# Performance work log

Hardware: AMD Instinct MI355X
Metric: run time of the kernel (lower is better)

The kernel has to match this reference:

```python
import jax, jax.numpy as jnp
import numpy as np

B, S, D = 2, 2048, 1024
H = 16
HD = D // H  # 64


def setup_inputs() -> dict:
    key = jax.random.key(0)
    ks = jax.random.split(key, 9)
    s = 1.0 / np.sqrt(D)
    return {
        "query_input": jax.random.normal(ks[0], (B, S, D), dtype=jnp.float32),
        "Wq": jax.random.normal(ks[1], (D, D), dtype=jnp.float32) * s,
        "bq": jax.random.normal(ks[2], (D,), dtype=jnp.float32) * 0.02,
        "Wk": jax.random.normal(ks[3], (D, D), dtype=jnp.float32) * s,
        "bk": jax.random.normal(ks[4], (D,), dtype=jnp.float32) * 0.02,
        "Wv": jax.random.normal(ks[5], (D, D), dtype=jnp.float32) * s,
        "bv": jax.random.normal(ks[6], (D,), dtype=jnp.float32) * 0.02,
        "Wo": jax.random.normal(ks[7], (D, D), dtype=jnp.float32) * s,
        "bo": jax.random.normal(ks[8], (D,), dtype=jnp.float32) * 0.02,
    }


def _split_heads(x):
    # [B, S, D] -> [B, H, S, HD]
    return x.reshape(B, S, H, HD).transpose(0, 2, 1, 3)


def reference(query_input, Wq, bq, Wk, bk, Wv, bv, Wo, bo):
    # self-attention: key_value_input = query_input
    q = _split_heads(query_input @ Wq + bq)
    k = _split_heads(query_input @ Wk + bk)
    v = _split_heads(query_input @ Wv + bv)
    scores = jnp.einsum("bhqd,bhkd->bhqk", q, k) / jnp.sqrt(jnp.float32(HD))
    probs = jax.nn.softmax(scores, axis=-1)  # dropout is identity in eval
    ctx = jnp.einsum("bhqk,bhkd->bhqd", probs, v)
    ctx = ctx.transpose(0, 2, 1, 3).reshape(B, S, D)
    return ctx @ Wo + bo
```

## Files before the change

kernel.cpp:

```cpp
#include <hip/hip_runtime.h>
#include <hip/hip_bf16.h>
#include <cstdint>

constexpr int Bsz = 2, Seq = 2048, Dim = 1024, NH = 16, HDim = 64;
constexpr int Mtok = Bsz * Seq;
constexpr int NQKV = 3 * Dim;
constexpr float QSCALE = 0.125f * 1.4426950408889634f;

typedef __attribute__((ext_vector_type(4))) float f32x4;
typedef __attribute__((ext_vector_type(16))) float f32x16;
typedef __attribute__((ext_vector_type(8))) short bf16x8;

#if __has_builtin(__builtin_amdgcn_exp2f)
#define EXP2(x) __builtin_amdgcn_exp2f(x)
#else
#define EXP2(x) exp2f(x)
#endif

__device__ __forceinline__ ushort f2bf(float f) {
    union { float f; uint32_t u; } v; v.f = f;
    uint32_t u = v.u;
    uint32_t r = (u + 0x7fffu + ((u >> 16) & 1u)) >> 16;
    return (ushort)r;
}

__device__ __forceinline__ uint cvt_pk_bf16(float lo, float hi) {
    uint r;
    asm("v_cvt_pk_bf16_f32 %0, %1, %2" : "=v"(r) : "v"(lo), "v"(hi));
    return r;
}

__device__ __forceinline__ void gll16(const ushort* g, ushort* l) {
    __builtin_amdgcn_global_load_lds(
        (const __attribute__((address_space(1))) void*)g,
        (__attribute__((address_space(3))) void*)l, 16, 0, 0);
}

__global__ void convert_x(const float* __restrict__ in, ushort* __restrict__ out, int n16) {
    int i = blockIdx.x * 256 + threadIdx.x;
    if (i >= n16) return;
    int e = i * 16;
    int row = e >> 10;
    int k = e & 1023;
    int k0 = k & ~31;
    int c = (k >> 3) & 3;
    int sw = row & 3;
    const float4* p = (const float4*)(in + e);
    float4 a = p[0], b = p[1], c2 = p[2], d = p[3];
    uint4 o0, o1;
    o0.x = (uint)f2bf(a.x) | ((uint)f2bf(a.y) << 16);
    o0.y = (uint)f2bf(a.z) | ((uint)f2bf(a.w) << 16);
    o0.z = (uint)f2bf(b.x) | ((uint)f2bf(b.y) << 16);
    o0.w = (uint)f2bf(b.z) | ((uint)f2bf(b.w) << 16);
    o1.x = (uint)f2bf(c2.x) | ((uint)f2bf(c2.y) << 16);
    o1.y = (uint)f2bf(c2.z) | ((uint)f2bf(c2.w) << 16);
    o1.z = (uint)f2bf(d.x) | ((uint)f2bf(d.y) << 16);
    o1.w = (uint)f2bf(d.z) | ((uint)f2bf(d.w) << 16);
    ushort* dstrow = out + (size_t)row * 1024 + k0;
    *(uint4*)(dstrow + ((c ^ sw) << 3))       = o0;
    *(uint4*)(dstrow + (((c + 1) ^ sw) << 3)) = o1;
}

__global__ void transpose_w4(const float* __restrict__ Wq, const float* __restrict__ Wk,
                             const float* __restrict__ Wv, const float* __restrict__ Wo,
                             ushort* __restrict__ Wtqkv, ushort* __restrict__ Wto) {
    __shared__ float tile[32][33];
    int z = blockIdx.z;
    const float* src = (z == 0) ? Wq : (z == 1) ? Wk : (z == 2) ? Wv : Wo;
    ushort* dst = (z == 3) ? Wto : Wtqkv + (size_t)z * 1024 * 1024;
    float scale = (z == 0) ? QSCALE : 1.f;
    int bx = blockIdx.x * 32, by = blockIdx.y * 32;
    int tx = threadIdx.x, ty = threadIdx.y;
#pragma unroll
    for (int j = 0; j < 32; j += 8)
        tile[ty + j][tx] = src[(size_t)(by + ty + j) * Dim + bx + tx];
    __syncthreads();
    int c = tx >> 3, wn8 = tx & 7;
#pragma unroll
    for (int j = 0; j < 32; j += 8) {
        int n = bx + ty + j;
        dst[(size_t)n * Dim + by + ((c ^ (n & 3)) << 3) + wn8] = f2bf(tile[tx][ty + j] * scale);
    }
}

__global__ void concat_bias(const float* __restrict__ bq, const float* __restrict__ bk,
                            const float* __restrict__ bv, float* __restrict__ dst) {
    int i = blockIdx.x * 256 + threadIdx.x;
    if (i >= NQKV) return;
    float v = (i < 1024) ? bq[i] * QSCALE : (i < 2048 ? bk[i - 1024] : bv[i - 2048]);
    dst[i] = v;
}

__global__ __launch_bounds__(256) void gemm_qkv(const ushort* __restrict__ A,
                                                const ushort* __restrict__ Bt,
                                                const float* __restrict__ bias,
                                                ushort* __restrict__ Qp,
                                                ushort* __restrict__ Kp,
                                                ushort* __restrict__ Vp) {
    __shared__ ushort As[2][128 * 32];
    __shared__ ushort Bs[2][128 * 32];
    const int tid = threadIdx.x;
    const int lane = tid & 63, wid = tid >> 6;
    const int wm = wid >> 1, wn = wid & 1;
    const int bm = blockIdx.x * 128, bn = blockIdx.y * 128;
    const int g = lane >> 4, r16 = lane & 15;
    const int Ksz = Dim;

    f32x4 acc[4][4] = {};

    const int srow = tid >> 2;
    const int sc = tid & 3;
    const ushort* ga0 = A + (size_t)(bm + srow) * Ksz + sc * 8;
    const ushort* ga1 = A + (size_t)(bm + 64 + srow) * Ksz + sc * 8;
    const ushort* gb0 = Bt + (size_t)(bn + srow) * Ksz + sc * 8;
    const ushort* gb1 = Bt + (size_t)(bn + 64 + srow) * Ksz + sc * 8;
    const int lofs = wid << 9;

#define GSTAGE(bufi, k_)  do {                          \
        gll16(ga0 + (k_), &As[bufi][lofs]);             \
        gll16(ga1 + (k_), &As[bufi][2048 + lofs]);      \
        gll16(gb0 + (k_), &Bs[bufi][lofs]);             \
        gll16(gb1 + (k_), &Bs[bufi][2048 + lofs]);      \
    } while (0)

    GSTAGE(0, 0);
    int cur = 0;

    for (int k0 = 0; k0 < Ksz; k0 += 32) {
        __syncthreads();
        if (k0 + 32 < Ksz) GSTAGE(cur ^ 1, k0 + 32);
        const ushort* Asb = As[cur];
        const ushort* Bsb = Bs[cur];
        bf16x8 af[4], bfr[4];
#pragma unroll
        for (int mt = 0; mt < 4; mt++) {
            int row = wm * 64 + mt * 16 + r16;
            af[mt] = *(const bf16x8*)(Asb + row * 32 + ((g ^ (row & 3)) * 8));
        }
#pragma unroll
        for (int nt = 0; nt < 4; nt++) {
            int row = wn * 64 + nt * 16 + r16;
            bfr[nt] = *(const bf16x8*)(Bsb + row * 32 + ((g ^ (row & 3)) * 8));
        }
#pragma unroll
        for (int mt = 0; mt < 4; mt++)
#pragma unroll
            for (int nt = 0; nt < 4; nt++)
                acc[mt][nt] = __builtin_amdgcn_mfma_f32_16x16x32_bf16(af[mt], bfr[nt], acc[mt][nt], 0, 0, 0);
        cur ^= 1;
    }
#undef GSTAGE

#pragma unroll
    for (int nt = 0; nt < 4; nt++) {
        int col = bn + wn * 64 + nt * 16 + r16;
        float bv = bias[col];
        if (col < 1024) {
#pragma unroll
            for (int mt = 0; mt < 4; mt++) {
                int row0 = bm + wm * 64 + mt * 16 + g * 4;
                f32x4 c = acc[mt][nt];
#pragma unroll
                for (int i = 0; i < 4; i++)
                    Qp[(size_t)(row0 + i) * 1024 + col] = f2bf(c[i] + bv);
            }
        } else if (col < 2048) {
            int h = (col - 1024) >> 6, d = (col - 1024) & 63;
#pragma unroll
            for (int mt = 0; mt < 4; mt++) {
                int row0 = bm + wm * 64 + mt * 16 + g * 4;
                f32x4 c = acc[mt][nt];
#pragma unroll
                for (int i = 0; i < 4; i++) {
                    int row = row0 + i;
                    int b = row >> 11, s = row & 2047;
                    size_t idx = ((size_t)(b * 16 + h) * 2048 + s) * 64
                               + (((d >> 3) ^ (s & 7)) << 3) + (d & 7);
                    Kp[idx] = f2bf(c[i] + bv);
                }
            }
        } else {
            int h = (col - 2048) >> 6, dv = (col - 2048) & 63;
#pragma unroll
            for (int mt = 0; mt < 4; mt++) {
                int row0 = bm + wm * 64 + mt * 16 + g * 4;
                f32x4 c = acc[mt][nt];
                int b = row0 >> 11, s = row0 & 2047;
                int s0 = s & ~63, si = s & 63;
                uint2 pk;
                pk.x = cvt_pk_bf16(c[0] + bv, c[1] + bv);
                pk.y = cvt_pk_bf16(c[2] + bv, c[3] + bv);
                size_t idx = ((size_t)(b * 16 + h) * 2048 + s0) * 64 + dv * 64
                           + (((si >> 3) ^ (dv & 7)) << 3) + (si & 7);
                *(uint2*)(Vp + idx) = pk;
            }
        }
    }
}

__global__ __launch_bounds__(256) void gemm_bt(const ushort* __restrict__ A,
                                               const ushort* __restrict__ Bt,
                                               const float* __restrict__ bias,
                                               float* __restrict__ Cout,
                                               int Nsz, int Ksz) {
    __shared__ ushort As[2][128 * 32];
    __shared__ ushort Bs[2][128 * 32];
    const int tid = threadIdx.x;
    const int lane = tid & 63, wid = tid >> 6;
    const int wm = wid >> 1, wn = wid & 1;
    const int bm = blockIdx.x * 128, bn = blockIdx.y * 128;
    const int g = lane >> 4, r16 = lane & 15;

    f32x4 acc[4][4] = {};

    const int srow = tid >> 2;
    const int sc = tid & 3;
    const ushort* ga0 = A + (size_t)(bm + srow) * Ksz + sc * 8;
    const ushort* ga1 = A + (size_t)(bm + 64 + srow) * Ksz + sc * 8;
    const ushort* gb0 = Bt + (size_t)(bn + srow) * Ksz + sc * 8;
    const ushort* gb1 = Bt + (size_t)(bn + 64 + srow) * Ksz + sc * 8;
    const int lofs = wid << 9;

#define GSTAGE(bufi, k_)  do {                          \
        gll16(ga0 + (k_), &As[bufi][lofs]);             \
        gll16(ga1 + (k_), &As[bufi][2048 + lofs]);      \
        gll16(gb0 + (k_), &Bs[bufi][lofs]);             \
        gll16(gb1 + (k_), &Bs[bufi][2048 + lofs]);      \
    } while (0)

    GSTAGE(0, 0);
    int cur = 0;

    for (int k0 = 0; k0 < Ksz; k0 += 32) {
        __syncthreads();
        if (k0 + 32 < Ksz) GSTAGE(cur ^ 1, k0 + 32);
        const ushort* Asb = As[cur];
        const ushort* Bsb = Bs[cur];
        bf16x8 af[4], bfr[4];
#pragma unroll
        for (int mt = 0; mt < 4; mt++) {
            int row = wm * 64 + mt * 16 + r16;
            af[mt] = *(const bf16x8*)(Asb + row * 32 + ((g ^ (row & 3)) * 8));
        }
#pragma unroll
        for (int nt = 0; nt < 4; nt++) {
            int row = wn * 64 + nt * 16 + r16;
            bfr[nt] = *(const bf16x8*)(Bsb + row * 32 + ((g ^ (row & 3)) * 8));
        }
#pragma unroll
        for (int mt = 0; mt < 4; mt++)
#pragma unroll
            for (int nt = 0; nt < 4; nt++)
                acc[mt][nt] = __builtin_amdgcn_mfma_f32_16x16x32_bf16(af[mt], bfr[nt], acc[mt][nt], 0, 0, 0);
        cur ^= 1;
    }
#undef GSTAGE

#pragma unroll
    for (int nt = 0; nt < 4; nt++) {
        int col = bn + wn * 64 + nt * 16 + r16;
        float bv = bias[col];
#pragma unroll
        for (int mt = 0; mt < 4; mt++) {
            int row0 = bm + wm * 64 + mt * 16 + g * 4;
            f32x4 c = acc[mt][nt];
#pragma unroll
            for (int i = 0; i < 4; i++)
                Cout[(size_t)(row0 + i) * Nsz + col] = c[i] + bv;
        }
    }
}

__global__ __launch_bounds__(256) void attn(const ushort* __restrict__ Qp,
                                            const ushort* __restrict__ Kp,
                                            const ushort* __restrict__ Vp,
                                            ushort* __restrict__ Ctx) {
    __shared__ ushort Ks[2][64 * 64];
    __shared__ ushort Vs[2][64 * 64];
    __shared__ float Rl[4][32];
    const int tid = threadIdx.x, lane = tid & 63, w = tid >> 6;
    const int bh = blockIdx.y, b = bh >> 4, h = bh & 15;
    const int l31 = lane & 31, hi = lane >> 5, sw7 = l31 & 7;
    const bool lo = (hi == 0);
    const int qrow = blockIdx.x * 128 + w * 32;

    const ushort* Qr = Qp + (size_t)(b * Seq + qrow + l31) * 1024 + h * 64;
    bf16x8 qf[4];
#pragma unroll
    for (int ks = 0; ks < 4; ks++)
        qf[ks] = *(const bf16x8*)(Qr + ks * 16 + hi * 8);

    const ushort* KpB = Kp + (size_t)bh * Seq * 64;
    const ushort* VpB = Vp + (size_t)bh * Seq * 64;
    const int wb = w * 512;

#define STAGE(bufi, kv0_)  do {                                        \
        const ushort* ks_ = KpB + (size_t)(kv0_) * 64 + tid * 8;       \
        const ushort* vs_ = VpB + (size_t)(kv0_) * 64 + tid * 8;       \
        gll16(ks_,        &Ks[bufi][wb]);                              \
        gll16(ks_ + 2048, &Ks[bufi][2048 + wb]);                       \
        gll16(vs_,        &Vs[bufi][wb]);                              \
        gll16(vs_ + 2048, &Vs[bufi][2048 + wb]);                       \
    } while (0)

    STAGE(0, 0);

    f32x16 c0 = {}, c1 = {};
    float l_run = 0.f;
    int cur = 0;

    for (int kv0 = 0; kv0 < Seq; kv0 += 64) {
        __syncthreads();
        if (kv0 + 64 < Seq) STAGE(cur ^ 1, kv0 + 64);
        const ushort* Kt = Ks[cur];
        const ushort* Vt = Vs[cur];

        f32x16 s0, s1;
#pragma unroll
        for (int r = 0; r < 16; r++) { s0[r] = -8.f; s1[r] = -8.f; }
        __builtin_amdgcn_s_setprio(1);
#pragma unroll
        for (int ks = 0; ks < 4; ks++) {
            int ch = ((ks * 2 + hi) ^ sw7) << 3;
            bf16x8 k0 = *(const bf16x8*)(Kt + l31 * 64 + ch);
            bf16x8 k1 = *(const bf16x8*)(Kt + (32 + l31) * 64 + ch);
            s0 = __builtin_amdgcn_mfma_f32_32x32x16_bf16(k0, qf[ks], s0, 0, 0, 0);
            s1 = __builtin_amdgcn_mfma_f32_32x32x16_bf16(k1, qf[ks], s1, 0, 0, 0);
        }
        __builtin_amdgcn_s_setprio(0);

        float p0[16], p1[16];
        float ls0 = 0.f, ls1 = 0.f;
#pragma unroll
        for (int r = 0; r < 16; r++) {
            p0[r] = EXP2(s0[r]);
            p1[r] = EXP2(s1[r]);
            ls0 += p0[r]; ls1 += p1[r];
        }
        l_run += ls0 + ls1;

        bf16x8 pa[4];
#pragma unroll
        for (int sl = 0; sl < 4; sl++) {
            const float* pp = (sl < 2) ? p0 : p1;
            int rb = (sl & 1) * 8;
            uint x  = cvt_pk_bf16(pp[rb + 0], pp[rb + 1]);
            uint x2 = cvt_pk_bf16(pp[rb + 2], pp[rb + 3]);
            uint y  = cvt_pk_bf16(pp[rb + 4], pp[rb + 5]);
            uint y2 = cvt_pk_bf16(pp[rb + 6], pp[rb + 7]);
            asm("v_permlane32_swap_b32 %0, %1" : "+v"(x),  "+v"(y));
            asm("v_permlane32_swap_b32 %0, %1" : "+v"(x2), "+v"(y2));
            union { uint u[4]; bf16x8 v; } fr;
            fr.u[0] = x;
            fr.u[1] = x2;
            fr.u[2] = y;
            fr.u[3] = y2;
            pa[sl] = fr.v;
        }

        __builtin_amdgcn_s_setprio(1);
#pragma unroll
        for (int sl = 0; sl < 4; sl++) {
            int ch = ((sl * 2 + hi) ^ sw7) << 3;
            bf16x8 vf0 = *(const bf16x8*)(Vt + l31 * 64 + ch);
            bf16x8 vf1 = *(const bf16x8*)(Vt + (32 + l31) * 64 + ch);
            c0 = __builtin_amdgcn_mfma_f32_32x32x16_bf16(pa[sl], vf0, c0, 0, 0, 0);
            c1 = __builtin_amdgcn_mfma_f32_32x32x16_bf16(pa[sl], vf1, c1, 0, 0, 0);
        }
        __builtin_amdgcn_s_setprio(0);
        cur ^= 1;
    }
#undef STAGE

    float lt = l_run + __shfl_xor(l_run, 32);
    if (lo) Rl[w][l31] = 1.f / lt;
    __builtin_amdgcn_s_waitcnt(0);
    float rlv[16];
#pragma unroll
    for (int r = 0; r < 16; r++)
        rlv[r] = Rl[w][(r & 3) + 8 * (r >> 2) + 4 * hi];

    const int rowbase = b * Seq + qrow;
    const int cl = l31 >> 3, c7 = l31 & 7;
#pragma unroll
    for (int r = 0; r < 16; r++) {
        int q = (r & 3) + 8 * (r >> 2) + 4 * hi;
        int row = rowbase + q;
        int col0 = h * 64 + ((cl ^ (row & 3)) << 3) + c7;
        int col1 = h * 64 + 32 + ((cl ^ (row & 3)) << 3) + c7;
        Ctx[(size_t)row * Dim + col0] = f2bf(c0[r] * rlv[r]);
        Ctx[(size_t)row * Dim + col1] = f2bf(c1[r] * rlv[r]);
    }
}

extern "C" void kernel_launch(void* const* d_in, const int* in_sizes, int n_in,
                              void* d_out, int out_size, void* d_ws, size_t ws_size,
                              hipStream_t stream) {
    const float* X  = (const float*)d_in[0];
    const float* Wq = (const float*)d_in[1];
    const float* bq = (const float*)d_in[2];
    const float* Wk = (const float*)d_in[3];
    const float* bk = (const float*)d_in[4];
    const float* Wv = (const float*)d_in[5];
    const float* bv = (const float*)d_in[6];
    const float* Wo = (const float*)d_in[7];
    const float* bo = (const float*)d_in[8];

    char* ws = (char*)d_ws;
    ushort* Xb    = (ushort*)(ws);
    ushort* Wtqkv = (ushort*)(ws + 8388608);
    ushort* Wto   = (ushort*)(ws + 14680064);
    float*  bqkv  = (float*)(ws + 16777216);
    ushort* Qp    = (ushort*)(ws + 16793600);
    ushort* Kp    = (ushort*)(ws + 25182208);
    ushort* Vp    = (ushort*)(ws + 33570816);
    ushort* Ctxb  = (ushort*)(ws + 41959424);

    convert_x<<<1024, 256, 0, stream>>>(X, Xb, Mtok * Dim / 16);
    transpose_w4<<<dim3(32, 32, 4), dim3(32, 8), 0, stream>>>(Wq, Wk, Wv, Wo, Wtqkv, Wto);
    concat_bias<<<12, 256, 0, stream>>>(bq, bk, bv, bqkv);

    gemm_qkv<<<dim3(32, 24), 256, 0, stream>>>(Xb, Wtqkv, bqkv, Qp, Kp, Vp);
    attn<<<dim3(16, 32), 256, 0, stream>>>(Qp, Kp, Vp, Ctxb);
    gemm_bt<<<dim3(32, 8), 256, 0, stream>>>(Ctxb, Wto, bo, (float*)d_out, Dim, Dim);
}
```

Baseline: 130.6 us.

## Rewrite QKV GEMM with 256x256 tiles, 8 waves, and interleaved load/MFMA schedule

The QKV projection GEMM now uses 256x256 block tiles with 512 threads and a 64-wide K step. Global-to-LDS loads are split into A and B halves and issued between MFMA phases, with explicit barriers, priority hints and vmcnt waits. The XOR swizzle that producers used to apply to stored data is removed and applied instead on the global-load side of the GEMMs, so producers write plain row-major output. Larger tiles raise data reuse and cut the block count, but the grid of 192 blocks may underfill the GPU and raise register pressure.

After: 127.8 us. 2.1% less time.

```diff
diff --git a/kernel.cpp b/kernel.cpp
--- a/kernel.cpp
+++ b/kernel.cpp
@@ -39,13 +39,7 @@
 __global__ void convert_x(const float* __restrict__ in, ushort* __restrict__ out, int n16) {
     int i = blockIdx.x * 256 + threadIdx.x;
     if (i >= n16) return;
-    int e = i * 16;
-    int row = e >> 10;
-    int k = e & 1023;
-    int k0 = k & ~31;
-    int c = (k >> 3) & 3;
-    int sw = row & 3;
-    const float4* p = (const float4*)(in + e);
+    const float4* p = (const float4*)in + (size_t)i * 4;
     float4 a = p[0], b = p[1], c2 = p[2], d = p[3];
     uint4 o0, o1;
     o0.x = (uint)f2bf(a.x) | ((uint)f2bf(a.y) << 16);
@@ -56,9 +50,9 @@
     o1.y = (uint)f2bf(c2.z) | ((uint)f2bf(c2.w) << 16);
     o1.z = (uint)f2bf(d.x) | ((uint)f2bf(d.y) << 16);
     o1.w = (uint)f2bf(d.z) | ((uint)f2bf(d.w) << 16);
-    ushort* dstrow = out + (size_t)row * 1024 + k0;
-    *(uint4*)(dstrow + ((c ^ sw) << 3))       = o0;
-    *(uint4*)(dstrow + (((c + 1) ^ sw) << 3)) = o1;
+    uint4* dst = (uint4*)out + (size_t)i * 2;
+    dst[0] = o0;
+    dst[1] = o1;
 }
 
 __global__ void transpose_w4(const float* __restrict__ Wq, const float* __restrict__ Wk,
@@ -75,11 +69,10 @@
     for (int j = 0; j < 32; j += 8)
         tile[ty + j][tx] = src[(size_t)(by + ty + j) * Dim + bx + tx];
     __syncthreads();
-    int c = tx >> 3, wn8 = tx & 7;
 #pragma unroll
     for (int j = 0; j < 32; j += 8) {
         int n = bx + ty + j;
-        dst[(size_t)n * Dim + by + ((c ^ (n & 3)) << 3) + wn8] = f2bf(tile[tx][ty + j] * scale);
+        dst[(size_t)n * Dim + by + tx] = f2bf(tile[tx][ty + j] * scale);
     }
 }
 
@@ -91,85 +84,133 @@
     dst[i] = v;
 }
 
-__global__ __launch_bounds__(256) void gemm_qkv(const ushort* __restrict__ A,
-                                                const ushort* __restrict__ Bt,
-                                                const float* __restrict__ bias,
-                                                ushort* __restrict__ Qp,
-                                                ushort* __restrict__ Kp,
-                                                ushort* __restrict__ Vp) {
-    __shared__ ushort As[2][128 * 32];
-    __shared__ ushort Bs[2][128 * 32];
+__global__ __launch_bounds__(512, 2) void gemm_qkv(const ushort* __restrict__ A,
+                                                   const ushort* __restrict__ Bt,
+                                                   const float* __restrict__ bias,
+                                                   ushort* __restrict__ Qp,
+                                                   ushort* __restrict__ Kp,
+                                                   ushort* __restrict__ Vp) {
+    __shared__ ushort Al[2][2][8192];
+    __shared__ ushort Bl[2][2][8192];
     const int tid = threadIdx.x;
     const int lane = tid & 63, wid = tid >> 6;
-    const int wm = wid >> 1, wn = wid & 1;
-    const int bm = blockIdx.x * 128, bn = blockIdx.y * 128;
+    const int wm = wid >> 2, wn = wid & 3;
     const int g = lane >> 4, r16 = lane & 15;
-    const int Ksz = Dim;
-
-    f32x4 acc[4][4] = {};
-
-    const int srow = tid >> 2;
-    const int sc = tid & 3;
-    const ushort* ga0 = A + (size_t)(bm + srow) * Ksz + sc * 8;
-    const ushort* ga1 = A + (size_t)(bm + 64 + srow) * Ksz + sc * 8;
-    const ushort* gb0 = Bt + (size_t)(bn + srow) * Ksz + sc * 8;
-    const ushort* gb1 = Bt + (size_t)(bn + 64 + srow) * Ksz + sc * 8;
-    const int lofs = wid << 9;
-
-#define GSTAGE(bufi, k_)  do {                          \
-        gll16(ga0 + (k_), &As[bufi][lofs]);             \
-        gll16(ga1 + (k_), &As[bufi][2048 + lofs]);      \
-        gll16(gb0 + (k_), &Bs[bufi][lofs]);             \
-        gll16(gb1 + (k_), &Bs[bufi][2048 + lofs]);      \
+    const int sw = r16 & 7;
+    const int bm = blockIdx.x * 256, bn = blockIdx.y * 256;
+    const int srow = tid >> 3;
+    const int gch = (tid & 7) ^ (srow & 7);
+    const int wofs = wid * 512;
+
+    const ushort* gAb = A  + (size_t)(bm + srow) * 1024 + gch * 8;
+    const ushort* gBb = Bt + (size_t)(bn + srow) * 1024 + gch * 8;
+
+#define STAGE_A(buf, h, t) do {                                          \
+        const ushort* s_ = gAb + (size_t)(h) * 131072 + (t) * 64;        \
+        gll16(s_,         &Al[buf][h][wofs]);                            \
+        gll16(s_ + 65536, &Al[buf][h][4096 + wofs]);                     \
     } while (0)
-
-    GSTAGE(0, 0);
-    int cur = 0;
-
-    for (int k0 = 0; k0 < Ksz; k0 += 32) {
-        __syncthreads();
-        if (k0 + 32 < Ksz) GSTAGE(cur ^ 1, k0 + 32);
-        const ushort* Asb = As[cur];
-        const ushort* Bsb = Bs[cur];
-        bf16x8 af[4], bfr[4];
-#pragma unroll
-        for (int mt = 0; mt < 4; mt++) {
-            int row = wm * 64 + mt * 16 + r16;
-            af[mt] = *(const bf16x8*)(Asb + row * 32 + ((g ^ (row & 3)) * 8));
-        }
-#pragma unroll
-        for (int nt = 0; nt < 4; nt++) {
-            int row = wn * 64 + nt * 16 + r16;
-            bfr[nt] = *(const bf16x8*)(Bsb + row * 32 + ((g ^ (row & 3)) * 8));
-        }
-#pragma unroll
-        for (int mt = 0; mt < 4; mt++)
-#pragma unroll
-            for (int nt = 0; nt < 4; nt++)
-                acc[mt][nt] = __builtin_amdgcn_mfma_f32_16x16x32_bf16(af[mt], bfr[nt], acc[mt][nt], 0, 0, 0);
-        cur ^= 1;
-    }
-#undef GSTAGE
-
-#pragma unroll
-    for (int nt = 0; nt < 4; nt++) {
-        int col = bn + wn * 64 + nt * 16 + r16;
-        float bv = bias[col];
-        if (col < 1024) {
-#pragma unroll
-            for (int mt = 0; mt < 4; mt++) {
-                int row0 = bm + wm * 64 + mt * 16 + g * 4;
-                f32x4 c = acc[mt][nt];
+#define STAGE_B(buf, h, t) do {                                          \
+        const ushort* s_ = gBb + (size_t)(h) * 131072 + (t) * 64;        \
+        gll16(s_,         &Bl[buf][h][wofs]);                            \
+        gll16(s_ + 65536, &Bl[buf][h][4096 + wofs]);                     \
+    } while (0)
+#define LDA(buf, mi, ks) (*(const bf16x8*)&Al[buf][wm][((mi)*16 + r16) * 64 + ((((ks)*4 + g) ^ sw) * 8)])
+#define LDB(buf, ni, ks) (*(const bf16x8*)&Bl[buf][wn >> 1][((wn & 1) * 64 + (ni)*16 + r16) * 64 + ((((ks)*4 + g) ^ sw) * 8)])
+
+    f32x4 acc[8][4] = {};
+    bf16x8 a0[4][2], a1[4][2], bA[2][2], bB[2][2];
+
+    STAGE_A(0, 0, 0); STAGE_A(0, 1, 0); STAGE_B(0, 0, 0); STAGE_B(0, 1, 0);
+    STAGE_A(1, 0, 1); STAGE_A(1, 1, 1); STAGE_B(1, 0, 1); STAGE_B(1, 1, 1);
+    asm volatile("s_waitcnt vmcnt(8)" ::: "memory");
+    __builtin_amdgcn_s_barrier();
+    __builtin_amdgcn_sched_barrier(0);
+
+#pragma unroll 2
+    for (int t = 0; t < 16; ++t) {
+        const int buf = t & 1;
+#pragma unroll
+        for (int mi = 0; mi < 4; mi++) { a0[mi][0] = LDA(buf, mi, 0); a0[mi][1] = LDA(buf, mi, 1); }
+#pragma unroll
+        for (int ni = 0; ni < 2; ni++) { bA[ni][0] = LDB(buf, ni, 0); bA[ni][1] = LDB(buf, ni, 1); }
+        __builtin_amdgcn_s_setprio(1);
+#pragma unroll
+        for (int mi = 0; mi < 4; mi++)
+#pragma unroll
+            for (int ni = 0; ni < 2; ni++)
+#pragma unroll
+                for (int ks = 0; ks < 2; ks++)
+                    acc[mi][ni] = __builtin_amdgcn_mfma_f32_16x16x32_bf16(a0[mi][ks], bA[ni][ks], acc[mi][ni], 0, 0, 0);
+        __builtin_amdgcn_s_setprio(0);
+#pragma unroll
+        for (int ni = 0; ni < 2; ni++) { bB[ni][0] = LDB(buf, 2 + ni, 0); bB[ni][1] = LDB(buf, 2 + ni, 1); }
+        __builtin_amdgcn_s_setprio(1);
+#pragma unroll
+        for (int mi = 0; mi < 4; mi++)
+#pragma unroll
+            for (int ni = 0; ni < 2; ni++)
+#pragma unroll
+                for (int ks = 0; ks < 2; ks++)
+                    acc[mi][2 + ni] = __builtin_amdgcn_mfma_f32_16x16x32_bf16(a0[mi][ks], bB[ni][ks], acc[mi][2 + ni], 0, 0, 0);
+        __builtin_amdgcn_s_setprio(0);
+        __builtin_amdgcn_s_barrier();
+        __builtin_amdgcn_sched_barrier(0);
+#pragma unroll
+        for (int mi = 0; mi < 4; mi++) { a1[mi][0] = LDA(buf, 4 + mi, 0); a1[mi][1] = LDA(buf, 4 + mi, 1); }
+        if (t + 2 < 16) { STAGE_B(buf, 0, t + 2); STAGE_B(buf, 1, t + 2); }
+        __builtin_amdgcn_s_setprio(1);
+#pragma unroll
+        for (int mi = 0; mi < 4; mi++)
+#pragma unroll
+            for (int ni = 0; ni < 2; ni++)
+#pragma unroll
+                for (int ks = 0; ks < 2; ks++)
+                    acc[4 + mi][2 + ni] = __builtin_amdgcn_mfma_f32_16x16x32_bf16(a1[mi][ks], bB[ni][ks], acc[4 + mi][2 + ni], 0, 0, 0);
+        __builtin_amdgcn_s_setprio(0);
+        __builtin_amdgcn_s_barrier();
+        __builtin_amdgcn_sched_barrier(0);
+        if (t + 2 < 16) { STAGE_A(buf, 0, t + 2); STAGE_A(buf, 1, t + 2); }
+        __builtin_amdgcn_s_setprio(1);
+#pragma unroll
+        for (int mi = 0; mi < 4; mi++)
+#pragma unroll
+            for (int ni = 0; ni < 2; ni++)
+#pragma unroll
+                for (int ks = 0; ks < 2; ks++)
+                    acc[4 + mi][ni] = __builtin_amdgcn_mfma_f32_16x16x32_bf16(a1[mi][ks], bA[ni][ks], acc[4 + mi][ni], 0, 0, 0);
+        __builtin_amdgcn_s_setprio(0);
+        if (t + 2 < 16) asm volatile("s_waitcnt vmcnt(8)" ::: "memory");
+        else            asm volatile("s_waitcnt vmcnt(0)" ::: "memory");
+        __builtin_amdgcn_s_barrier();
+        __builtin_amdgcn_sched_barrier(0);
+    }
+#undef STAGE_A
+#undef STAGE_B
+#undef LDA
+#undef LDB
+
+    const int by = blockIdx.y;
+#pragma unroll
+    for (int ni = 0; ni < 4; ni++) {
+        const int col = bn + wn * 64 + ni * 16 + r16;
+        const float bv = bias[col];
+        if (by < 4) {
+#pragma unroll
+            for (int mi = 0; mi < 8; mi++) {
+                int row0 = bm + wm * 128 + mi * 16 + g * 4;
+                f32x4 c = acc[mi][ni];
 #pragma unroll
                 for (int i = 0; i < 4; i++)
                     Qp[(size_t)(row0 + i) * 1024 + col] = f2bf(c[i] + bv);
             }
-        } else if (col < 2048) {
-            int h = (col - 1024) >> 6, d = (col - 1024) & 63;
-#pragma unroll
-            for (int mt = 0; mt < 4; mt++) {
-                int row0 = bm + wm * 64 + mt * 16 + g * 4;
-                f32x4 c = acc[mt][nt];
+        } else if (by < 8) {
+            int h = ((bn - 1024) >> 6) + wn;
+            int d = ni * 16 + r16;
+#pragma unroll
+            for (int mi = 0; mi < 8; mi++) {
+                int row0 = bm + wm * 128 + mi * 16 + g * 4;
+                f32x4 c = acc[mi][ni];
 #pragma unroll
                 for (int i = 0; i < 4; i++) {
                     int row = row0 + i;
@@ -180,11 +221,12 @@
                 }
             }
         } else {
-            int h = (col - 2048) >> 6, dv = (col - 2048) & 63;
-#pragma unroll
-            for (int mt = 0; mt < 4; mt++) {
-                int row0 = bm + wm * 64 + mt * 16 + g * 4;
-                f32x4 c = acc[mt][nt];
+            int h = ((bn - 2048) >> 6) + wn;
+            int dv = ni * 16 + r16;
+#pragma unroll
+            for (int mi = 0; mi < 8; mi++) {
+                int row0 = bm + wm * 128 + mi * 16 + g * 4;
+                f32x4 c = acc[mi][ni];
                 int b = row0 >> 11, s = row0 & 2047;
                 int s0 = s & ~63, si = s & 63;
                 uint2 pk;
@@ -214,7 +256,7 @@
     f32x4 acc[4][4] = {};
 
     const int srow = tid >> 2;
-    const int sc = tid & 3;
+    const int sc = (tid & 3) ^ (srow & 3);
     const ushort* ga0 = A + (size_t)(bm + srow) * Ksz + sc * 8;
     const ushort* ga1 = A + (size_t)(bm + 64 + srow) * Ksz + sc * 8;
     const ushort* gb0 = Bt + (size_t)(bn + srow) * Ksz + sc * 8;
@@ -381,15 +423,12 @@
         rlv[r] = Rl[w][(r & 3) + 8 * (r >> 2) + 4 * hi];
 
     const int rowbase = b * Seq + qrow;
-    const int cl = l31 >> 3, c7 = l31 & 7;
 #pragma unroll
     for (int r = 0; r < 16; r++) {
         int q = (r & 3) + 8 * (r >> 2) + 4 * hi;
         int row = rowbase + q;
-        int col0 = h * 64 + ((cl ^ (row & 3)) << 3) + c7;
-        int col1 = h * 64 + 32 + ((cl ^ (row & 3)) << 3) + c7;
-        Ctx[(size_t)row * Dim + col0] = f2bf(c0[r] * rlv[r]);
-        Ctx[(size_t)row * Dim + col1] = f2bf(c1[r] * rlv[r]);
+        Ctx[(size_t)row * Dim + h * 64 + l31]      = f2bf(c0[r] * rlv[r]);
+        Ctx[(size_t)row * Dim + h * 64 + 32 + l31] = f2bf(c1[r] * rlv[r]);
     }
 }
 
@@ -420,7 +459,7 @@
     transpose_w4<<<dim3(32, 32, 4), dim3(32, 8), 0, stream>>>(Wq, Wk, Wv, Wo, Wtqkv, Wto);
     concat_bias<<<12, 256, 0, stream>>>(bq, bk, bv, bqkv);
 
-    gemm_qkv<<<dim3(32, 24), 256, 0, stream>>>(Xb, Wtqkv, bqkv, Qp, Kp, Vp);
+    gemm_qkv<<<dim3(16, 12), 512, 0, stream>>>(Xb, Wtqkv, bqkv, Qp, Kp, Vp);
     attn<<<dim3(16, 32), 256, 0, stream>>>(Qp, Kp, Vp, Ctxb);
     gemm_bt<<<dim3(32, 8), 256, 0, stream>>>(Ctxb, Wto, bo, (float*)d_out, Dim, Dim);
 }
```
